# Kernel tuning notes

Measured on AMD Instinct MI355X. Metric: run time of the kernel, lower is better.

Reference implementation:

```python
import jax, jax.numpy as jnp
import numpy as np

C = 10000   # crystals
K = 5       # elements per crystal
N = C * K   # nodes
EMB = 200   # element embedding length
F = 64      # elem_fea_len
L = 3       # n_graph
H = 3       # heads
HID = 256   # gate/msg hidden dim


def setup_inputs() -> dict:
    key = jax.random.key(0)
    ks = jax.random.split(key, 16)
    # structured intra-crystal all-pairs edge lists (grouped by crystal)
    i_loc = np.repeat(np.arange(K), K)
    j_loc = np.tile(np.arange(K), K)
    base = np.arange(C)[:, None] * K
    self_idx = (base + i_loc).ravel().astype(np.int32)   # [M]
    nbr_idx = (base + j_loc).ravel().astype(np.int32)    # [M]
    cry_idx = np.repeat(np.arange(C), K).astype(np.int32)  # [N]
    def nrm(k, shape, s=0.05):
        return jax.random.normal(k, shape, jnp.float32) * s
    return dict(
        elem_weights=jax.random.uniform(ks[0], (N, 1), jnp.float32, 0.05, 1.0),
        elem_fea=jax.random.normal(ks[1], (N, EMB), jnp.float32),
        self_fea_idx=jnp.asarray(self_idx),
        nbr_fea_idx=jnp.asarray(nbr_idx),
        cry_elem_idx=jnp.asarray(cry_idx),
        n_crystals=C,
        emb_W=nrm(ks[2], (EMB, F - 1)), emb_b=jnp.zeros((F - 1,), jnp.float32),
        g_gate_W1=nrm(ks[3], (L, H, 2 * F, HID)), g_gate_b1=jnp.zeros((L, H, HID), jnp.float32),
        g_gate_W2=nrm(ks[4], (L, H, HID, 1)), g_gate_b2=jnp.zeros((L, H, 1), jnp.float32),
        g_msg_W1=nrm(ks[5], (L, H, 2 * F, HID)), g_msg_b1=jnp.zeros((L, H, HID), jnp.float32),
        g_msg_W2=nrm(ks[6], (L, H, HID, F)), g_msg_b2=jnp.zeros((L, H, F), jnp.float32),
        g_pow=jax.random.normal(ks[7], (L, H), jnp.float32),
        c_gate_W1=nrm(ks[8], (H, F, HID)), c_gate_b1=jnp.zeros((H, HID), jnp.float32),
        c_gate_W2=nrm(ks[9], (H, HID, 1)), c_gate_b2=jnp.zeros((H, 1), jnp.float32),
        c_msg_W1=nrm(ks[10], (H, F, HID)), c_msg_b1=jnp.zeros((H, HID), jnp.float32),
        c_msg_W2=nrm(ks[11], (H, HID, F)), c_msg_b2=jnp.zeros((H, F), jnp.float32),
        c_pow=jax.random.normal(ks[12], (H,), jnp.float32),
    )


def _simple(h, W1, b1, W2, b2):
    # SimpleNetwork: Linear -> LeakyReLU -> Linear (one hidden layer, slope 0.01)
    return jax.nn.leaky_relu(h @ W1 + b1, 0.01) @ W2 + b2


def _attn(fea, weights, index, nseg, gW1, gb1, gW2, gb2, mW1, mb1, mW2, mb2, p):
    # WeightedAttention: segment softmax with learned power on weights
    gate = _simple(fea, gW1, gb1, gW2, gb2)                                   # [E,1]
    gate = gate - jax.ops.segment_max(gate, index, num_segments=nseg)[index]
    gate = weights ** p * jnp.exp(gate)
    gate = gate / (jax.ops.segment_sum(gate, index, num_segments=nseg)[index] + 1e-10)
    msg = _simple(fea, mW1, mb1, mW2, mb2)                                    # [E,F]
    return jax.ops.segment_sum(gate * msg, index, num_segments=nseg)          # [nseg,F]


_attn_heads = jax.vmap(_attn, in_axes=(None, None, None, None, 0, 0, 0, 0, 0, 0, 0, 0, 0))


def _forward(elem_weights, elem_fea, self_fea_idx, nbr_fea_idx, cry_elem_idx, n_crystals,
             emb_W, emb_b,
             g_gate_W1, g_gate_b1, g_gate_W2, g_gate_b2,
             g_msg_W1, g_msg_b1, g_msg_W2, g_msg_b2, g_pow,
             c_gate_W1, c_gate_b1, c_gate_W2, c_gate_b2,
             c_msg_W1, c_msg_b1, c_msg_W2, c_msg_b2, c_pow):
    n_nodes = elem_fea.shape[0]
    x = jnp.concatenate([elem_fea @ emb_W + emb_b, elem_weights], axis=1)     # [N,F]
    w_nbr = elem_weights[nbr_fea_idx]                                          # [M,1]
    for l in range(g_pow.shape[0]):  # n_graph message layers
        cat = jnp.concatenate([x[self_fea_idx], x[nbr_fea_idx]], axis=1)      # [M,2F]
        heads = _attn_heads(cat, w_nbr, self_fea_idx, n_nodes,
                            g_gate_W1[l], g_gate_b1[l], g_gate_W2[l], g_gate_b2[l],
                            g_msg_W1[l], g_msg_b1[l], g_msg_W2[l], g_msg_b2[l], g_pow[l])
        x = heads.mean(0) + x
    heads = _attn_heads(x, elem_weights, cry_elem_idx, n_crystals,
                        c_gate_W1, c_gate_b1, c_gate_W2, c_gate_b2,
                        c_msg_W1, c_msg_b1, c_msg_W2, c_msg_b2, c_pow)
    return heads.mean(0)                                                       # [C,F]


def reference(elem_weights, elem_fea, self_fea_idx, nbr_fea_idx, cry_elem_idx, n_crystals,
              emb_W, emb_b,
              g_gate_W1, g_gate_b1, g_gate_W2, g_gate_b2,
              g_msg_W1, g_msg_b1, g_msg_W2, g_msg_b2, g_pow,
              c_gate_W1, c_gate_b1, c_gate_W2, c_gate_b2,
              c_msg_W1, c_msg_b1, c_msg_W2, c_msg_b2, c_pow):
    return _forward(elem_weights, elem_fea, self_fea_idx, nbr_fea_idx, cry_elem_idx, n_crystals,
                    emb_W, emb_b,
                    g_gate_W1, g_gate_b1, g_gate_W2, g_gate_b2,
                    g_msg_W1, g_msg_b1, g_msg_W2, g_msg_b2, g_pow,
                    c_gate_W1, c_gate_b1, c_gate_W2, c_gate_b2,
                    c_msg_W1, c_msg_b1, c_msg_W2, c_msg_b2, c_pow)
```

## Files before the change

kernel.cpp:

```cpp
#include <hip/hip_runtime.h>
#include <hip/hip_bf16.h>

#define K 5
#define F 64
#define EMBD 200
#define HID 256
#define NH 3
#define NL 3

#define CW 3
#define NWN (CW * K)
#define EWE (CW * K * K)
#define ET 5

typedef _Float16 half8 __attribute__((ext_vector_type(8)));
typedef _Float16 h2 __attribute__((ext_vector_type(2)));
typedef _Float16 h4 __attribute__((ext_vector_type(4)));
typedef __fp16 fp16x2 __attribute__((ext_vector_type(2)));
typedef float f32x4 __attribute__((ext_vector_type(4)));

__device__ __forceinline__ float lrelu(float v) { return v >= 0.f ? v : 0.01f * v; }

__device__ __forceinline__ h2 cvt_pk(float a, float b) {
    union { fp16x2 f; h2 h; } u;
    u.f = __builtin_amdgcn_cvt_pkrtz(a, b);
    return u.h;
}

__device__ __forceinline__ half8 lrelu8(half8 t) {
    half8 z = 0;
    half8 p = __builtin_elementwise_max(t, z);
    half8 n = __builtin_elementwise_min(t, z);
    return p + n * (_Float16)0.01f;
}

#define W1SW_ELEMS 589824
#define W2SW_ELEMS 147456
#define CW1_ELEMS   98304
#define CW2_ELEMS   49152
#define WALL_ELEMS (W1SW_ELEMS + W2SW_ELEMS + CW1_ELEMS + CW2_ELEMS)

#define W1L_ELEMS 196608
#define W2L_ELEMS 49152

__global__ __launch_bounds__(256)
void prep_all(const float* __restrict__ gW1, const float* __restrict__ mW1,
              const float* __restrict__ mW2,
              const float* __restrict__ cgW1, const float* __restrict__ cmW1,
              const float* __restrict__ cmW2,
              _Float16* __restrict__ Wall)
{
    int tid = blockIdx.x * 256 + threadIdx.x;
    if (tid >= WALL_ELEMS) return;
    float v;
    if (tid < W1SW_ELEMS) {
        int j = tid & 7, lane = (tid >> 3) & 63;
        int r1 = tid >> 9;
        int ks = r1 & 1, nt = (r1 >> 1) & 3, chunk = (r1 >> 3) & 3;
        int half = (r1 >> 5) & 1, net = (r1 >> 6) & 1, lh = r1 >> 7;
        int q = lane >> 4, n16 = lane & 15;
        const float* src = net ? mW1 : gW1;
        v = src[((size_t)lh * 128 + half * 64 + ks * 32 + q * 8 + j) * 256
                + chunk * 64 + nt * 16 + n16];
    } else if (tid < W1SW_ELEMS + W2SW_ELEMS) {
        int t2 = tid - W1SW_ELEMS;
        int j = t2 & 7, lane = (t2 >> 3) & 63;
        int r1 = t2 >> 9;
        int nt = r1 & 3, ks2 = (r1 >> 2) & 7, lh = r1 >> 5;
        int q = lane >> 4, n16 = lane & 15;
        v = mW2[((size_t)lh * 256 + ks2 * 32 + q * 8 + j) * 64 + nt * 16 + n16];
    } else if (tid < W1SW_ELEMS + W2SW_ELEMS + CW1_ELEMS) {
        int t2 = tid - (W1SW_ELEMS + W2SW_ELEMS);
        int j = t2 & 7, lane = (t2 >> 3) & 63;
        int r1 = t2 >> 9;
        int ks = r1 & 1, nt = (r1 >> 1) & 3, chunk = (r1 >> 3) & 3;
        int net = (r1 >> 5) & 1, h = r1 >> 6;
        int q = lane >> 4, n16 = lane & 15;
        const float* src = net ? cmW1 : cgW1;
        v = src[((size_t)h * 64 + ks * 32 + q * 8 + j) * 256
                + chunk * 64 + nt * 16 + n16];
    } else {
        int t2 = tid - (W1SW_ELEMS + W2SW_ELEMS + CW1_ELEMS);
        int j = t2 & 7, lane = (t2 >> 3) & 63;
        int r1 = t2 >> 9;
        int nt = r1 & 3, ks2 = (r1 >> 2) & 7, h = r1 >> 5;
        int q = lane >> 4, n16 = lane & 15;
        v = cmW2[((size_t)h * 256 + ks2 * 32 + q * 8 + j) * 64 + nt * 16 + n16];
    }
    Wall[tid] = (_Float16)v;
}

__global__ __launch_bounds__(256)
void prep_layer(const float* __restrict__ gW1, const float* __restrict__ mW1,
                const float* __restrict__ mW2,
                _Float16* __restrict__ W1sw, _Float16* __restrict__ W2sw, int l)
{
    int tid = blockIdx.x * 256 + threadIdx.x;
    if (tid < W1L_ELEMS) {
        int j = tid & 7, lane = (tid >> 3) & 63;
        int r1 = tid >> 9;
        int ks = r1 & 1, nt = (r1 >> 1) & 3, chunk = (r1 >> 3) & 3;
        int half = (r1 >> 5) & 1, net = (r1 >> 6) & 1, hh = r1 >> 7;
        int q = lane >> 4, n16 = lane & 15;
        const float* src = net ? mW1 : gW1;
        float v = src[((size_t)(l * NH + hh) * 128 + half * 64 + ks * 32 + q * 8 + j) * 256
                      + chunk * 64 + nt * 16 + n16];
        W1sw[tid] = (_Float16)v;
    } else {
        int t2 = tid - W1L_ELEMS;
        if (t2 < W2L_ELEMS) {
            int j = t2 & 7, lane = (t2 >> 3) & 63;
            int r1 = t2 >> 9;
            int nt = r1 & 3, ks2 = (r1 >> 2) & 7, hh = r1 >> 5;
            int q = lane >> 4, n16 = lane & 15;
            float v = mW2[((size_t)(l * NH + hh) * 256 + ks2 * 32 + q * 8 + j) * 64
                          + nt * 16 + n16];
            W2sw[t2] = (_Float16)v;
        }
    }
}

__global__ __launch_bounds__(64)
void embed_kernel(const float* __restrict__ fea, const float* __restrict__ W,
                  const float* __restrict__ b, const float* __restrict__ wts,
                  float* __restrict__ x)
{
    int n = blockIdx.x;
    int o = threadIdx.x;
    __shared__ float fs[EMBD];
    for (int e = o; e < EMBD; e += 64) fs[e] = fea[n * EMBD + e];
    __syncthreads();
    if (o < F - 1) {
        float acc = b[o];
#pragma unroll 8
        for (int e = 0; e < EMBD; ++e) acc += fs[e] * W[e * (F - 1) + o];
        x[n * F + o] = acc;
    } else {
        x[n * F + F - 1] = wts[n];
    }
}

#define WAVE_LDS 12288

__global__ __launch_bounds__(256, 2)
void net_wave(const float* __restrict__ x,
              const _Float16* __restrict__ W1sw,
              const _Float16* __restrict__ W2sw,
              const float* __restrict__ gb1, const float* __restrict__ gb2v,
              const float* __restrict__ mb1, const float* __restrict__ mb2,
              const float* __restrict__ gW2, const float* __restrict__ gpw,
              const _Float16* __restrict__ cW1sw,
              const _Float16* __restrict__ cW2sw,
              const float* __restrict__ cgb1, const float* __restrict__ cgb2v,
              const float* __restrict__ cmb1, const float* __restrict__ cmb2,
              const float* __restrict__ cgW2, const float* __restrict__ cpw,
              const float* __restrict__ wts, float* __restrict__ out, int Ntot)
{
    __shared__ __align__(16) char smem[4 * WAVE_LDS];

    const int t = threadIdx.x, w = t >> 6, lane = t & 63;
    const int q = lane >> 4, m16 = lane & 15;

    char* wb = smem + w * WAVE_LDS;
    _Float16 (*PQ)[16][72] = (_Float16 (*)[16][72])wb;
    _Float16 (*msgL)[72]   = (_Float16 (*)[72])wb;
    _Float16 (*xS)[72]     = (_Float16 (*)[72])(wb + 9216);
    float* gateS  = (float*)(wb + 11520);
    float* anormS = (float*)(wb + 11840);
    float* wpowS  = (float*)(wb + 12160);

    const int nw0 = (blockIdx.x * 12 + w * CW) * K;
    const int c0  = blockIdx.x * 12 + w * CW;
    const int Ctot = Ntot / K;
    const int vn  = (Ntot - nw0 < NWN) ? (Ntot - nw0) : NWN;
    const int vc  = (Ctot - c0 < CW) ? (Ctot - c0) : CW;
    (void)vn;

    half8 A[2];
    {
        int arow = nw0 + m16;
        if (arow > Ntot - 1) arow = Ntot - 1;
        if (arow < 0) arow = 0;
        const float* xr = x + (size_t)arow * F;
#pragma unroll
        for (int ks = 0; ks < 2; ++ks) {
            float4 f0 = *(const float4*)(xr + ks * 32 + q * 8);
            float4 f1 = *(const float4*)(xr + ks * 32 + q * 8 + 4);
            half8 a;
            a[0] = (_Float16)f0.x; a[1] = (_Float16)f0.y;
            a[2] = (_Float16)f0.z; a[3] = (_Float16)f0.w;
            a[4] = (_Float16)f1.x; a[5] = (_Float16)f1.y;
            a[6] = (_Float16)f1.z; a[7] = (_Float16)f1.w;
            A[ks] = a;
        }
    }

    float xcur[NWN];
#pragma unroll
    for (int n = 0; n < NWN; ++n) {
        int r = nw0 + n;
        if (r > Ntot - 1) r = Ntot - 1;
        if (r < 0) r = 0;
        xcur[n] = x[(size_t)r * F + lane];
    }

    int iR[ET], jR[ET];
#pragma unroll
    for (int et = 0; et < ET; ++et) {
        int e = et * 16 + m16;
        if (e < EWE) {
            int cl = e / 25, rm = e % 25;
            iR[et] = cl * K + rm / K;
            jR[et] = cl * K + rm % K;
        } else { iR[et] = 15; jR[et] = 15; }
    }

#pragma clang loop unroll(disable)
    for (int l = 0; l < NL; ++l) {
        float oacc[NWN];
#pragma unroll
        for (int n = 0; n < NWN; ++n) oacc[n] = 0.f;

        for (int h = 0; h < NH; ++h) {
            const int lh = l * NH + h, lhw = lh;

            if (lane < NWN) {
                int wi = nw0 + lane;
                if (wi > Ntot - 1) wi = Ntot - 1;
                if (wi < 0) wi = 0;
                wpowS[lane] = powf(wts[wi], gpw[lh]);
            }
            if (lane >= NWN && lane < NWN + 5) anormS[EWE + (lane - NWN)] = 0.f;

            f32x4 acc2[ET][4];
#pragma unroll
            for (int et = 0; et < ET; ++et)
#pragma unroll
                for (int nt = 0; nt < 4; ++nt) acc2[et][nt] = (f32x4){0.f, 0.f, 0.f, 0.f};
            float gacc[ET] = {0.f, 0.f, 0.f, 0.f, 0.f};

            for (int c = 0; c < 4; ++c) {
                half8 B2[8];
                {
                    const _Float16* W2b = W2sw + ((size_t)lhw * 8 + c * 2) * 2048;
#pragma unroll
                    for (int f = 0; f < 8; ++f)
                        B2[f] = *(const half8*)(W2b + ((size_t)f * 64 + lane) * 8);
                }

#pragma unroll
                for (int hf = 0; hf < 4; ++hf) {
                    f32x4 accS[4];
#pragma unroll
                    for (int nt = 0; nt < 4; ++nt) accS[nt] = (f32x4){0.f, 0.f, 0.f, 0.f};
                    const _Float16* Wb = W1sw + ((size_t)lhw * 4 + hf) * 16384 + c * 4096;
#pragma unroll
                    for (int nt = 0; nt < 4; ++nt)
#pragma unroll
                        for (int ks = 0; ks < 2; ++ks) {
                            half8 B = *(const half8*)(Wb + ((nt * 2 + ks) * 64 + lane) * 8);
                            accS[nt] = __builtin_amdgcn_mfma_f32_16x16x32_f16(
                                B, A[ks], accS[nt], 0, 0, 0);
                        }
#pragma unroll
                    for (int nt = 0; nt < 4; ++nt) {
                        h2 lo = cvt_pk(accS[nt][0], accS[nt][1]);
                        h2 hi = cvt_pk(accS[nt][2], accS[nt][3]);
                        h4 pk = __builtin_shufflevector(lo, hi, 0, 1, 2, 3);
                        *(h4*)&PQ[hf][m16][nt * 16 + q * 4] = pk;
                    }
                }

                half8 bg8[2], bm8[2];
                h2 wgh2[2][4];
#pragma unroll
                for (int ks = 0; ks < 2; ++ks) {
                    const int ub = c * 64 + ks * 32 + q * 8;
                    float4 g0 = *(const float4*)(gb1 + (size_t)lh * HID + ub);
                    float4 g1 = *(const float4*)(gb1 + (size_t)lh * HID + ub + 4);
                    float4 m0 = *(const float4*)(mb1 + (size_t)lh * HID + ub);
                    float4 m1 = *(const float4*)(mb1 + (size_t)lh * HID + ub + 4);
                    float4 w0 = *(const float4*)(gW2 + (size_t)lh * HID + ub);
                    float4 w1 = *(const float4*)(gW2 + (size_t)lh * HID + ub + 4);
                    half8 bg, bm;
                    bg[0]=(_Float16)g0.x; bg[1]=(_Float16)g0.y; bg[2]=(_Float16)g0.z; bg[3]=(_Float16)g0.w;
                    bg[4]=(_Float16)g1.x; bg[5]=(_Float16)g1.y; bg[6]=(_Float16)g1.z; bg[7]=(_Float16)g1.w;
                    bm[0]=(_Float16)m0.x; bm[1]=(_Float16)m0.y; bm[2]=(_Float16)m0.z; bm[3]=(_Float16)m0.w;
                    bm[4]=(_Float16)m1.x; bm[5]=(_Float16)m1.y; bm[6]=(_Float16)m1.z; bm[7]=(_Float16)m1.w;
                    bg8[ks] = bg; bm8[ks] = bm;
                    wgh2[ks][0] = cvt_pk(w0.x, w0.y);
                    wgh2[ks][1] = cvt_pk(w0.z, w0.w);
                    wgh2[ks][2] = cvt_pk(w1.x, w1.y);
                    wgh2[ks][3] = cvt_pk(w1.z, w1.w);
                }

#pragma unroll
                for (int et = 0; et < ET; ++et) {
                    half8 af[2];
#pragma unroll
                    for (int ks = 0; ks < 2; ++ks) {
                        const int ub = ks * 32 + q * 8;
                        half8 pg = *(const half8*)&PQ[0][iR[et]][ub];
                        half8 qg = *(const half8*)&PQ[1][jR[et]][ub];
                        half8 pm = *(const half8*)&PQ[2][iR[et]][ub];
                        half8 qm = *(const half8*)&PQ[3][jR[et]][ub];
                        half8 tg = lrelu8(pg + qg + bg8[ks]);
                        h2 t01 = __builtin_shufflevector(tg, tg, 0, 1);
                        h2 t23 = __builtin_shufflevector(tg, tg, 2, 3);
                        h2 t45 = __builtin_shufflevector(tg, tg, 4, 5);
                        h2 t67 = __builtin_shufflevector(tg, tg, 6, 7);
                        gacc[et] = __builtin_amdgcn_fdot2(t01, wgh2[ks][0], gacc[et], false);
                        gacc[et] = __builtin_amdgcn_fdot2(t23, wgh2[ks][1], gacc[et], false);
                        gacc[et] = __builtin_amdgcn_fdot2(t45, wgh2[ks][2], gacc[et], false);
                        gacc[et] = __builtin_amdgcn_fdot2(t67, wgh2[ks][3], gacc[et], false);
                        af[ks] = lrelu8(pm + qm + bm8[ks]);
                    }
#pragma unroll
                    for (int nt = 0; nt < 4; ++nt)
#pragma unroll
                        for (int ks = 0; ks < 2; ++ks)
                            acc2[et][nt] = __builtin_amdgcn_mfma_f32_16x16x32_f16(
                                af[ks], B2[ks * 4 + nt], acc2[et][nt], 0, 0, 0);
                }
            }

            const float gb2s = gb2v[lh];
#pragma unroll
            for (int et = 0; et < ET; ++et) {
                float g = gacc[et];
                g += __shfl_xor(g, 16);
                g += __shfl_xor(g, 32);
                if (q == 0) gateS[et * 16 + m16] = g + gb2s;
            }

            if (lane < NWN) {
                const int cl5 = (lane / K) * K;
                float gg[K], mx = -1e30f;
#pragma unroll
                for (int jj = 0; jj < K; ++jj) {
                    gg[jj] = gateS[lane * K + jj];
                    mx = fmaxf(mx, gg[jj]);
                }
                float s = 0.f, wv[K];
#pragma unroll
                for (int jj = 0; jj < K; ++jj) {
                    wv[jj] = wpowS[cl5 + jj] * expf(gg[jj] - mx);
                    s += wv[jj];
                }
                float inv = 1.f / (s + 1e-10f) * (1.f / 3.f);
#pragma unroll
                for (int jj = 0; jj < K; ++jj) anormS[lane * K + jj] = wv[jj] * inv;
            }

            float b2v[4];
#pragma unroll
            for (int nt = 0; nt < 4; ++nt) b2v[nt] = mb2[(size_t)lh * F + nt * 16 + m16];
#pragma unroll
            for (int et = 0; et < ET; ++et) {
                f32x4 an = *(const f32x4*)&anormS[et * 16 + q * 4];
#pragma unroll
                for (int nt = 0; nt < 4; ++nt)
#pragma unroll
                    for (int rg = 0; rg < 4; ++rg) {
                        float v = (acc2[et][nt][rg] + b2v[nt]) * an[rg];
                        msgL[et * 16 + q * 4 + rg][nt * 16 + m16] = (_Float16)v;
                    }
            }

#pragma unroll
            for (int n = 0; n < NWN; ++n) {
                float s = 0.f;
#pragma unroll
                for (int jj = 0; jj < K; ++jj) s += (float)msgL[n * K + jj][lane];
                oacc[n] += s;
            }
        }

#pragma unroll
        for (int n = 0; n < NWN; ++n) {
            float xn = oacc[n] + xcur[n];
            xcur[n] = xn;
            xS[n][lane] = (_Float16)xn;
        }
        xS[15][lane] = (_Float16)0.f;
#pragma unroll
        for (int ks = 0; ks < 2; ++ks)
            A[ks] = *(const half8*)&xS[m16][ks * 32 + q * 8];
    }

    _Float16 (*PQp)[16][72] = (_Float16 (*)[16][72])wb;
    _Float16 (*msgP)[72]    = (_Float16 (*)[72])wb;

    float oaccP[CW] = {0.f, 0.f, 0.f};

    for (int h = 0; h < NH; ++h) {
        if (lane < NWN) {
            int wi = nw0 + lane;
            if (wi > Ntot - 1) wi = Ntot - 1;
            if (wi < 0) wi = 0;
            wpowS[lane] = powf(wts[wi], cpw[h]);
        }
        if (lane == NWN) anormS[15] = 0.f;

        f32x4 acc2[4];
#pragma unroll
        for (int nt = 0; nt < 4; ++nt) acc2[nt] = (f32x4){0.f, 0.f, 0.f, 0.f};
        float gacc = 0.f;

        for (int c = 0; c < 4; ++c) {
            half8 B2[8];
            {
                const _Float16* W2b = cW2sw + (size_t)h * 16384 + c * 4096;
#pragma unroll
                for (int f = 0; f < 8; ++f)
                    B2[f] = *(const half8*)(W2b + ((size_t)f * 64 + lane) * 8);
            }

#pragma unroll
            for (int net = 0; net < 2; ++net) {
                f32x4 accS[4];
#pragma unroll
                for (int nt = 0; nt < 4; ++nt) accS[nt] = (f32x4){0.f, 0.f, 0.f, 0.f};
                const _Float16* Wb = cW1sw + ((size_t)(h * 2 + net) * 4 + c) * 4096;
#pragma unroll
                for (int nt = 0; nt < 4; ++nt)
#pragma unroll
                    for (int ks = 0; ks < 2; ++ks) {
                        half8 B = *(const half8*)(Wb + ((nt * 2 + ks) * 64 + lane) * 8);
                        accS[nt] = __builtin_amdgcn_mfma_f32_16x16x32_f16(
                            B, A[ks], accS[nt], 0, 0, 0);
                    }
#pragma unroll
                for (int nt = 0; nt < 4; ++nt) {
                    h2 lo = cvt_pk(accS[nt][0], accS[nt][1]);
                    h2 hi = cvt_pk(accS[nt][2], accS[nt][3]);
                    h4 pk = __builtin_shufflevector(lo, hi, 0, 1, 2, 3);
                    *(h4*)&PQp[net][m16][nt * 16 + q * 4] = pk;
                }
            }

            half8 bg8[2], bm8[2];
            h2 wgh2[2][4];
#pragma unroll
            for (int ks = 0; ks < 2; ++ks) {
                const int ub = c * 64 + ks * 32 + q * 8;
                float4 g0 = *(const float4*)(cgb1 + (size_t)h * HID + ub);
                float4 g1 = *(const float4*)(cgb1 + (size_t)h * HID + ub + 4);
                float4 m0 = *(const float4*)(cmb1 + (size_t)h * HID + ub);
                float4 m1 = *(const float4*)(cmb1 + (size_t)h * HID + ub + 4);
                float4 w0 = *(const float4*)(cgW2 + (size_t)h * HID + ub);
                float4 w1 = *(const float4*)(cgW2 + (size_t)h * HID + ub + 4);
                half8 bg, bm;
                bg[0]=(_Float16)g0.x; bg[1]=(_Float16)g0.y; bg[2]=(_Float16)g0.z; bg[3]=(_Float16)g0.w;
                bg[4]=(_Float16)g1.x; bg[5]=(_Float16)g1.y; bg[6]=(_Float16)g1.z; bg[7]=(_Float16)g1.w;
                bm[0]=(_Float16)m0.x; bm[1]=(_Float16)m0.y; bm[2]=(_Float16)m0.z; bm[3]=(_Float16)m0.w;
                bm[4]=(_Float16)m1.x; bm[5]=(_Float16)m1.y; bm[6]=(_Float16)m1.z; bm[7]=(_Float16)m1.w;
                bg8[ks] = bg; bm8[ks] = bm;
                wgh2[ks][0] = cvt_pk(w0.x, w0.y);
                wgh2[ks][1] = cvt_pk(w0.z, w0.w);
                wgh2[ks][2] = cvt_pk(w1.x, w1.y);
                wgh2[ks][3] = cvt_pk(w1.z, w1.w);
            }

            {
                half8 af[2];
#pragma unroll
                for (int ks = 0; ks < 2; ++ks) {
                    const int ub = ks * 32 + q * 8;
                    half8 pg = *(const half8*)&PQp[0][m16][ub];
                    half8 pm = *(const half8*)&PQp[1][m16][ub];
                    half8 tg = lrelu8(pg + bg8[ks]);
                    h2 t01 = __builtin_shufflevector(tg, tg, 0, 1);
                    h2 t23 = __builtin_shufflevector(tg, tg, 2, 3);
                    h2 t45 = __builtin_shufflevector(tg, tg, 4, 5);
                    h2 t67 = __builtin_shufflevector(tg, tg, 6, 7);
                    gacc = __builtin_amdgcn_fdot2(t01, wgh2[ks][0], gacc, false);
                    gacc = __builtin_amdgcn_fdot2(t23, wgh2[ks][1], gacc, false);
                    gacc = __builtin_amdgcn_fdot2(t45, wgh2[ks][2], gacc, false);
                    gacc = __builtin_amdgcn_fdot2(t67, wgh2[ks][3], gacc, false);
                    af[ks] = lrelu8(pm + bm8[ks]);
                }
#pragma unroll
                for (int nt = 0; nt < 4; ++nt)
#pragma unroll
                    for (int ks = 0; ks < 2; ++ks)
                        acc2[nt] = __builtin_amdgcn_mfma_f32_16x16x32_f16(
                            af[ks], B2[ks * 4 + nt], acc2[nt], 0, 0, 0);
            }
        }

        const float gb2s = cgb2v[h];
        {
            float g = gacc;
            g += __shfl_xor(g, 16);
            g += __shfl_xor(g, 32);
            if (q == 0) gateS[m16] = g + gb2s;
        }

        if (lane < CW) {
            const int n0 = lane * K;
            float gg[K], mx = -1e30f;
#pragma unroll
            for (int jj = 0; jj < K; ++jj) {
                gg[jj] = gateS[n0 + jj];
                mx = fmaxf(mx, gg[jj]);
            }
            float s = 0.f, wv[K];
#pragma unroll
            for (int jj = 0; jj < K; ++jj) {
                wv[jj] = wpowS[n0 + jj] * expf(gg[jj] - mx);
                s += wv[jj];
            }
            float inv = 1.f / (s + 1e-10f) * (1.f / 3.f);
#pragma unroll
            for (int jj = 0; jj < K; ++jj) anormS[n0 + jj] = wv[jj] * inv;
        }

        float b2v[4];
#pragma unroll
        for (int nt = 0; nt < 4; ++nt) b2v[nt] = cmb2[(size_t)h * F + nt * 16 + m16];
#pragma unroll
        for (int nt = 0; nt < 4; ++nt)
#pragma unroll
            for (int rg = 0; rg < 4; ++rg) {
                int row = q * 4 + rg;
                float v = (acc2[nt][rg] + b2v[nt]) * anormS[row];
                msgP[row][nt * 16 + m16] = (_Float16)v;
            }

#pragma unroll
        for (int cl = 0; cl < CW; ++cl) {
            float s = 0.f;
#pragma unroll
            for (int jj = 0; jj < K; ++jj) s += (float)msgP[cl * K + jj][lane];
            oaccP[cl] += s;
        }
    }

#pragma unroll
    for (int cl = 0; cl < CW; ++cl)
        if (cl < vc)
            out[(size_t)(c0 + cl) * F + lane] = oaccP[cl];
}

__global__ __launch_bounds__(256, 2)
void layer_wave(float* __restrict__ x,
                const _Float16* __restrict__ W1sw,
                const _Float16* __restrict__ W2sw,
                const float* __restrict__ gb1, const float* __restrict__ gb2v,
                const float* __restrict__ mb1, const float* __restrict__ mb2,
                const float* __restrict__ gW2, const float* __restrict__ gpw,
                const float* __restrict__ wts, int l, int lhw0, int Ntot)
{
    __shared__ __align__(16) char smem[4 * WAVE_LDS];

    const int t = threadIdx.x, w = t >> 6, lane = t & 63;
    const int q = lane >> 4, m16 = lane & 15;

    char* wb = smem + w * WAVE_LDS;
    _Float16 (*PQ)[16][72] = (_Float16 (*)[16][72])wb;
    _Float16 (*msgL)[72]   = (_Float16 (*)[72])wb;
    float* gateS  = (float*)(wb + 11520);
    float* anormS = (float*)(wb + 11840);
    float* wpowS  = (float*)(wb + 12160);

    const int nw0 = (blockIdx.x * 12 + w * CW) * K;
    const int vn  = (Ntot - nw0 < NWN) ? (Ntot - nw0) : NWN;

    half8 A[2];
    {
        int arow = nw0 + m16;
        if (arow > Ntot - 1) arow = Ntot - 1;
        if (arow < 0) arow = 0;
        const float* xr = x + (size_t)arow * F;
#pragma unroll
        for (int ks = 0; ks < 2; ++ks) {
            float4 f0 = *(const float4*)(xr + ks * 32 + q * 8);
            float4 f1 = *(const float4*)(xr + ks * 32 + q * 8 + 4);
            half8 a;
            a[0] = (_Float16)f0.x; a[1] = (_Float16)f0.y;
            a[2] = (_Float16)f0.z; a[3] = (_Float16)f0.w;
            a[4] = (_Float16)f1.x; a[5] = (_Float16)f1.y;
            a[6] = (_Float16)f1.z; a[7] = (_Float16)f1.w;
            A[ks] = a;
        }
    }

    int iR[ET], jR[ET];
#pragma unroll
    for (int et = 0; et < ET; ++et) {
        int e = et * 16 + m16;
        if (e < EWE) {
            int cl = e / 25, rm = e % 25;
            iR[et] = cl * K + rm / K;
            jR[et] = cl * K + rm % K;
        } else { iR[et] = 15; jR[et] = 15; }
    }

    float oacc[NWN];
#pragma unroll
    for (int n = 0; n < NWN; ++n) oacc[n] = 0.f;

    for (int h = 0; h < NH; ++h) {
        const int lh = l * NH + h, lhw = lhw0 + h;

        if (lane < NWN) {
            int wi = nw0 + lane;
            if (wi > Ntot - 1) wi = Ntot - 1;
            if (wi < 0) wi = 0;
            wpowS[lane] = powf(wts[wi], gpw[lh]);
        }
        if (lane >= NWN && lane < NWN + 5) anormS[EWE + (lane - NWN)] = 0.f;

        f32x4 acc2[ET][4];
#pragma unroll
        for (int et = 0; et < ET; ++et)
#pragma unroll
            for (int nt = 0; nt < 4; ++nt) acc2[et][nt] = (f32x4){0.f, 0.f, 0.f, 0.f};
        float gacc[ET] = {0.f, 0.f, 0.f, 0.f, 0.f};

        for (int c = 0; c < 4; ++c) {
            half8 B2[8];
            {
                const _Float16* W2b = W2sw + ((size_t)lhw * 8 + c * 2) * 2048;
#pragma unroll
                for (int f = 0; f < 8; ++f)
                    B2[f] = *(const half8*)(W2b + ((size_t)f * 64 + lane) * 8);
            }

#pragma unroll
            for (int hf = 0; hf < 4; ++hf) {
                f32x4 accS[4];
#pragma unroll
                for (int nt = 0; nt < 4; ++nt) accS[nt] = (f32x4){0.f, 0.f, 0.f, 0.f};
                const _Float16* Wb = W1sw + ((size_t)lhw * 4 + hf) * 16384 + c * 4096;
#pragma unroll
                for (int nt = 0; nt < 4; ++nt)
#pragma unroll
                    for (int ks = 0; ks < 2; ++ks) {
                        half8 B = *(const half8*)(Wb + ((nt * 2 + ks) * 64 + lane) * 8);
                        accS[nt] = __builtin_amdgcn_mfma_f32_16x16x32_f16(
                            B, A[ks], accS[nt], 0, 0, 0);
                    }
#pragma unroll
                for (int nt = 0; nt < 4; ++nt) {
                    h2 lo = cvt_pk(accS[nt][0], accS[nt][1]);
                    h2 hi = cvt_pk(accS[nt][2], accS[nt][3]);
                    h4 pk = __builtin_shufflevector(lo, hi, 0, 1, 2, 3);
                    *(h4*)&PQ[hf][m16][nt * 16 + q * 4] = pk;
                }
            }

            half8 bg8[2], bm8[2];
            h2 wgh2[2][4];
#pragma unroll
            for (int ks = 0; ks < 2; ++ks) {
                const int ub = c * 64 + ks * 32 + q * 8;
                float4 g0 = *(const float4*)(gb1 + (size_t)lh * HID + ub);
                float4 g1 = *(const float4*)(gb1 + (size_t)lh * HID + ub + 4);
                float4 m0 = *(const float4*)(mb1 + (size_t)lh * HID + ub);
                float4 m1 = *(const float4*)(mb1 + (size_t)lh * HID + ub + 4);
                float4 w0 = *(const float4*)(gW2 + (size_t)lh * HID + ub);
                float4 w1 = *(const float4*)(gW2 + (size_t)lh * HID + ub + 4);
                half8 bg, bm;
                bg[0]=(_Float16)g0.x; bg[1]=(_Float16)g0.y; bg[2]=(_Float16)g0.z; bg[3]=(_Float16)g0.w;
                bg[4]=(_Float16)g1.x; bg[5]=(_Float16)g1.y; bg[6]=(_Float16)g1.z; bg[7]=(_Float16)g1.w;
                bm[0]=(_Float16)m0.x; bm[1]=(_Float16)m0.y; bm[2]=(_Float16)m0.z; bm[3]=(_Float16)m0.w;
                bm[4]=(_Float16)m1.x; bm[5]=(_Float16)m1.y; bm[6]=(_Float16)m1.z; bm[7]=(_Float16)m1.w;
                bg8[ks] = bg; bm8[ks] = bm;
                wgh2[ks][0] = cvt_pk(w0.x, w0.y);
                wgh2[ks][1] = cvt_pk(w0.z, w0.w);
                wgh2[ks][2] = cvt_pk(w1.x, w1.y);
                wgh2[ks][3] = cvt_pk(w1.z, w1.w);
            }

#pragma unroll
            for (int et = 0; et < ET; ++et) {
                half8 af[2];
#pragma unroll
                for (int ks = 0; ks < 2; ++ks) {
                    const int ub = ks * 32 + q * 8;
                    half8 pg = *(const half8*)&PQ[0][iR[et]][ub];
                    half8 qg = *(const half8*)&PQ[1][jR[et]][ub];
                    half8 pm = *(const half8*)&PQ[2][iR[et]][ub];
                    half8 qm = *(const half8*)&PQ[3][jR[et]][ub];
                    half8 tg = lrelu8(pg + qg + bg8[ks]);
                    h2 t01 = __builtin_shufflevector(tg, tg, 0, 1);
                    h2 t23 = __builtin_shufflevector(tg, tg, 2, 3);
                    h2 t45 = __builtin_shufflevector(tg, tg, 4, 5);
                    h2 t67 = __builtin_shufflevector(tg, tg, 6, 7);
                    gacc[et] = __builtin_amdgcn_fdot2(t01, wgh2[ks][0], gacc[et], false);
                    gacc[et] = __builtin_amdgcn_fdot2(t23, wgh2[ks][1], gacc[et], false);
                    gacc[et] = __builtin_amdgcn_fdot2(t45, wgh2[ks][2], gacc[et], false);
                    gacc[et] = __builtin_amdgcn_fdot2(t67, wgh2[ks][3], gacc[et], false);
                    af[ks] = lrelu8(pm + qm + bm8[ks]);
                }
#pragma unroll
                for (int nt = 0; nt < 4; ++nt)
#pragma unroll
                    for (int ks = 0; ks < 2; ++ks)
                        acc2[et][nt] = __builtin_amdgcn_mfma_f32_16x16x32_f16(
                            af[ks], B2[ks * 4 + nt], acc2[et][nt], 0, 0, 0);
            }
        }

        const float gb2s = gb2v[lh];
#pragma unroll
        for (int et = 0; et < ET; ++et) {
            float g = gacc[et];
            g += __shfl_xor(g, 16);
            g += __shfl_xor(g, 32);
            if (q == 0) gateS[et * 16 + m16] = g + gb2s;
        }

        if (lane < NWN) {
            const int cl5 = (lane / K) * K;
            float gg[K], mx = -1e30f;
#pragma unroll
            for (int jj = 0; jj < K; ++jj) {
                gg[jj] = gateS[lane * K + jj];
                mx = fmaxf(mx, gg[jj]);
            }
            float s = 0.f, wv[K];
#pragma unroll
            for (int jj = 0; jj < K; ++jj) {
                wv[jj] = wpowS[cl5 + jj] * expf(gg[jj] - mx);
                s += wv[jj];
            }
            float inv = 1.f / (s + 1e-10f) * (1.f / 3.f);
#pragma unroll
            for (int jj = 0; jj < K; ++jj) anormS[lane * K + jj] = wv[jj] * inv;
        }

        float b2v[4];
#pragma unroll
        for (int nt = 0; nt < 4; ++nt) b2v[nt] = mb2[(size_t)lh * F + nt * 16 + m16];
#pragma unroll
        for (int et = 0; et < ET; ++et) {
            f32x4 an = *(const f32x4*)&anormS[et * 16 + q * 4];
#pragma unroll
            for (int nt = 0; nt < 4; ++nt)
#pragma unroll
                for (int rg = 0; rg < 4; ++rg) {
                    float v = (acc2[et][nt][rg] + b2v[nt]) * an[rg];
                    msgL[et * 16 + q * 4 + rg][nt * 16 + m16] = (_Float16)v;
                }
        }

#pragma unroll
        for (int n = 0; n < NWN; ++n) {
            float s = 0.f;
#pragma unroll
            for (int jj = 0; jj < K; ++jj) s += (float)msgL[n * K + jj][lane];
            oacc[n] += s;
        }
    }

#pragma unroll
    for (int n = 0; n < NWN; ++n) {
        if (n < vn) {
            size_t idx = (size_t)(nw0 + n) * F + lane;
            x[idx] = oacc[n] + x[idx];
        }
    }
}

__global__ __launch_bounds__(256)
void pool_kernel(const float* __restrict__ x,
                 const float* __restrict__ cgW1, const float* __restrict__ cgb1,
                 const float* __restrict__ cgW2, const float* __restrict__ cgb2,
                 const float* __restrict__ cmW1, const float* __restrict__ cmb1,
                 const float* __restrict__ cmW2, const float* __restrict__ cmb2,
                 const float* __restrict__ cpw, const float* __restrict__ wts,
                 float* __restrict__ out)
{
    __shared__ float xs[K * F];
    __shared__ float hmS[K][HID];
    __shared__ float msgS[K][F];
    __shared__ float outacc[F];
    __shared__ float b1g[HID], b1m[HID], w2g[HID];
    __shared__ float b2mS[F];
    __shared__ float gpart[K][2];
    __shared__ float gate_s[K];
    __shared__ float anorm[K];
    __shared__ float wn[K], wpow[K];

    const int c = blockIdx.x;
    const int t = threadIdx.x;
    const int wave = t >> 6, lane = t & 63;

    for (int d = t; d < K * F; d += 256) xs[d] = x[c * K * F + d];
    if (t < F) outacc[t] = 0.f;
    if (t < K) wn[t] = wts[c * K + t];
    __syncthreads();

    for (int h = 0; h < NH; ++h) {
        if (t < HID) {
            b1g[t] = cgb1[(size_t)h * HID + t];
            b1m[t] = cmb1[(size_t)h * HID + t];
            w2g[t] = cgW2[(size_t)h * HID + t];
        }
        if (t < F) b2mS[t] = cmb2[(size_t)h * F + t];
        if (t < K) wpow[t] = powf(wn[t], cpw[h]);
        __syncthreads();

        {
            const int grp = t >> 7;
            const int up  = t & 127;
            const float* Wb = (grp == 0 ? cgW1 : cmW1) + (size_t)h * F * HID;
            const float2* W2p = (const float2*)Wb;
            float acc[K][2];
#pragma unroll
            for (int i = 0; i < K; ++i) { acc[i][0] = 0.f; acc[i][1] = 0.f; }
            for (int k = 0; k < F; ++k) {
                float2 wv = W2p[k * (HID / 2) + up];
#pragma unroll
                for (int i = 0; i < K; ++i) {
                    float xv = xs[i * F + k];
                    acc[i][0] += xv * wv.x;
                    acc[i][1] += xv * wv.y;
                }
            }
            if (grp == 0) {
#pragma unroll
                for (int i = 0; i < K; ++i) {
                    float h0 = lrelu(acc[i][0] + b1g[2 * up]);
                    float h1 = lrelu(acc[i][1] + b1g[2 * up + 1]);
                    float part = h0 * w2g[2 * up] + h1 * w2g[2 * up + 1];
#pragma unroll
                    for (int s = 32; s; s >>= 1) part += __shfl_xor(part, s);
                    if (lane == 0) gpart[i][wave & 1] = part;
                }
            } else {
#pragma unroll
                for (int i = 0; i < K; ++i) {
                    hmS[i][2 * up]     = lrelu(acc[i][0] + b1m[2 * up]);
                    hmS[i][2 * up + 1] = lrelu(acc[i][1] + b1m[2 * up + 1]);
                }
            }
        }
        __syncthreads();
        if (t < K) gate_s[t] = cgb2[h] + gpart[t][0] + gpart[t][1];

        {
            const float2* W232 = (const float2*)(cmW2 + (size_t)h * HID * F);
            if (t < K * (F / 2)) {
                int i  = t >> 5;
                int op = t & 31;
                float a0 = b2mS[2 * op], a1 = b2mS[2 * op + 1];
#pragma unroll 8
                for (int u = 0; u < HID; ++u) {
                    float2 wv = W232[u * (F / 2) + op];
                    float hv = hmS[i][u];
                    a0 += hv * wv.x;
                    a1 += hv * wv.y;
                }
                msgS[i][2 * op]     = a0;
                msgS[i][2 * op + 1] = a1;
            }
        }
        __syncthreads();

        if (t == 0) {
            float mx = -1e30f;
#pragma unroll
            for (int i = 0; i < K; ++i) mx = fmaxf(mx, gate_s[i]);
            float wv[K], s = 0.f;
#pragma unroll
            for (int i = 0; i < K; ++i) {
                wv[i] = wpow[i] * expf(gate_s[i] - mx);
                s += wv[i];
            }
            float inv = 1.f / (s + 1e-10f);
#pragma unroll
            for (int i = 0; i < K; ++i) anorm[i] = wv[i] * inv;
        }
        __syncthreads();

        if (t < F) {
            float s = 0.f;
#pragma unroll
            for (int i = 0; i < K; ++i) s += anorm[i] * msgS[i][t];
            outacc[t] += s * (1.f / 3.f);
        }
        __syncthreads();
    }

    if (t < F) out[(size_t)c * F + t] = outacc[t];
}

extern "C" void kernel_launch(void* const* d_in, const int* in_sizes, int n_in,
                              void* d_out, int out_size, void* d_ws, size_t ws_size,
                              hipStream_t stream)
{
    const float* wts  = (const float*)d_in[0];
    const float* fea  = (const float*)d_in[1];
    const float* embW = (const float*)d_in[6];
    const float* embB = (const float*)d_in[7];
    const float* gW1  = (const float*)d_in[8];
    const float* gb1  = (const float*)d_in[9];
    const float* gW2  = (const float*)d_in[10];
    const float* gb2  = (const float*)d_in[11];
    const float* mW1  = (const float*)d_in[12];
    const float* mb1  = (const float*)d_in[13];
    const float* mW2  = (const float*)d_in[14];
    const float* mb2  = (const float*)d_in[15];
    const float* gpw  = (const float*)d_in[16];
    const float* cgW1 = (const float*)d_in[17];
    const float* cgb1 = (const float*)d_in[18];
    const float* cgW2 = (const float*)d_in[19];
    const float* cgb2 = (const float*)d_in[20];
    const float* cmW1 = (const float*)d_in[21];
    const float* cmb1 = (const float*)d_in[22];
    const float* cmW2 = (const float*)d_in[23];
    const float* cmb2 = (const float*)d_in[24];
    const float* cpw  = (const float*)d_in[25];

    const int N = in_sizes[0];
    const int C = N / K;
    const int layer_blocks = (C + 11) / 12;

    float* x = (float*)d_ws;
    const size_t xbytes = (size_t)N * F * 4;
    const size_t need = xbytes + (size_t)WALL_ELEMS * 2;

    embed_kernel<<<N, 64, 0, stream>>>(fea, embW, embB, wts, x);

    if (ws_size >= need) {
        _Float16* Wall  = (_Float16*)((char*)d_ws + xbytes);
        _Float16* W1sw  = Wall;
        _Float16* W2sw  = Wall + W1SW_ELEMS;
        _Float16* cW1sw = Wall + W1SW_ELEMS + W2SW_ELEMS;
        _Float16* cW2sw = Wall + W1SW_ELEMS + W2SW_ELEMS + CW1_ELEMS;

        prep_all<<<(WALL_ELEMS + 255) / 256, 256, 0, stream>>>(
            gW1, mW1, mW2, cgW1, cmW1, cmW2, Wall);
        net_wave<<<layer_blocks, 256, 0, stream>>>(
            x, W1sw, W2sw, gb1, gb2, mb1, mb2, gW2, gpw,
            cW1sw, cW2sw, cgb1, cgb2, cmb1, cmb2, cgW2, cpw,
            wts, (float*)d_out, N);
    } else {
        _Float16* W1sw = (_Float16*)d_out;
        _Float16* W2sw = (_Float16*)((char*)d_out + 393216);
        for (int l = 0; l < NL; ++l) {
            prep_layer<<<(W1L_ELEMS + W2L_ELEMS) / 256, 256, 0, stream>>>(
                gW1, mW1, mW2, W1sw, W2sw, l);
            layer_wave<<<layer_blocks, 256, 0, stream>>>(x, W1sw, W2sw,
                                                         gb1, gb2, mb1, mb2, gW2, gpw, wts,
                                                         l, 0, N);
        }
        pool_kernel<<<C, 256, 0, stream>>>(x, cgW1, cgb1, cgW2, cgb2,
                                           cmW1, cmb1, cmW2, cmb2, cpw, wts,
                                           (float*)d_out);
    }
}
```

Measured before the change: 723.1 us.

## Fuse element embedding into net_wave using MFMA with pre-swizzled fp16 weights

Removes the separate embed_kernel launch on the fast path. The embedding matmul (200->63) now runs inside net_wave as fp16 MFMA, with a swizzled embedding weight block produced by prep_all. The result is staged in LDS and read back into the A fragments and xcur. This drops one launch plus the global write and re-read of x, but the embedding inputs now lose precision through fp16 rounding.

```diff
diff --git a/kernel.cpp b/kernel.cpp
--- a/kernel.cpp
+++ b/kernel.cpp
@@ -39,6 +39,8 @@
 #define CW1_ELEMS   98304
 #define CW2_ELEMS   49152
 #define WALL_ELEMS (W1SW_ELEMS + W2SW_ELEMS + CW1_ELEMS + CW2_ELEMS)
+#define EMBSW_ELEMS 14336
+#define WALL2_ELEMS (WALL_ELEMS + EMBSW_ELEMS)
 
 #define W1L_ELEMS 196608
 #define W2L_ELEMS 49152
@@ -47,11 +49,11 @@
 void prep_all(const float* __restrict__ gW1, const float* __restrict__ mW1,
               const float* __restrict__ mW2,
               const float* __restrict__ cgW1, const float* __restrict__ cmW1,
-              const float* __restrict__ cmW2,
+              const float* __restrict__ cmW2, const float* __restrict__ embW,
               _Float16* __restrict__ Wall)
 {
     int tid = blockIdx.x * 256 + threadIdx.x;
-    if (tid >= WALL_ELEMS) return;
+    if (tid >= WALL2_ELEMS) return;
     float v;
     if (tid < W1SW_ELEMS) {
         int j = tid & 7, lane = (tid >> 3) & 63;
@@ -79,13 +81,21 @@
         const float* src = net ? cmW1 : cgW1;
         v = src[((size_t)h * 64 + ks * 32 + q * 8 + j) * 256
                 + chunk * 64 + nt * 16 + n16];
-    } else {
+    } else if (tid < WALL_ELEMS) {
         int t2 = tid - (W1SW_ELEMS + W2SW_ELEMS + CW1_ELEMS);
         int j = t2 & 7, lane = (t2 >> 3) & 63;
         int r1 = t2 >> 9;
         int nt = r1 & 3, ks2 = (r1 >> 2) & 7, h = r1 >> 5;
         int q = lane >> 4, n16 = lane & 15;
         v = cmW2[((size_t)h * 256 + ks2 * 32 + q * 8 + j) * 64 + nt * 16 + n16];
+    } else {
+        int t2 = tid - WALL_ELEMS;
+        int j = t2 & 7, lane = (t2 >> 3) & 63;
+        int r1 = t2 >> 9;
+        int nt = r1 & 3, kk = r1 >> 2;
+        int q = lane >> 4, n16 = lane & 15;
+        int row = kk * 32 + q * 8 + j, col = nt * 16 + n16;
+        v = (row < EMBD && col < F - 1) ? embW[(size_t)row * (F - 1) + col] : 0.f;
     }
     Wall[tid] = (_Float16)v;
 }
@@ -141,9 +151,11 @@
 }
 
 #define WAVE_LDS 12288
+#define XFS 68
 
 __global__ __launch_bounds__(256, 2)
-void net_wave(const float* __restrict__ x,
+void net_wave(const float* __restrict__ fea, const float* __restrict__ embB,
+              const _Float16* __restrict__ embWsw,
               const _Float16* __restrict__ W1sw,
               const _Float16* __restrict__ W2sw,
               const float* __restrict__ gb1, const float* __restrict__ gb2v,
@@ -172,36 +184,60 @@
     const int nw0 = (blockIdx.x * 12 + w * CW) * K;
     const int c0  = blockIdx.x * 12 + w * CW;
     const int Ctot = Ntot / K;
-    const int vn  = (Ntot - nw0 < NWN) ? (Ntot - nw0) : NWN;
     const int vc  = (Ctot - c0 < CW) ? (Ctot - c0) : CW;
-    (void)vn;
-
-    half8 A[2];
+
+    float* xF = (float*)wb;
     {
         int arow = nw0 + m16;
         if (arow > Ntot - 1) arow = Ntot - 1;
         if (arow < 0) arow = 0;
-        const float* xr = x + (size_t)arow * F;
-#pragma unroll
-        for (int ks = 0; ks < 2; ++ks) {
-            float4 f0 = *(const float4*)(xr + ks * 32 + q * 8);
-            float4 f1 = *(const float4*)(xr + ks * 32 + q * 8 + 4);
-            half8 a;
-            a[0] = (_Float16)f0.x; a[1] = (_Float16)f0.y;
-            a[2] = (_Float16)f0.z; a[3] = (_Float16)f0.w;
-            a[4] = (_Float16)f1.x; a[5] = (_Float16)f1.y;
-            a[6] = (_Float16)f1.z; a[7] = (_Float16)f1.w;
-            A[ks] = a;
-        }
+        const float* fr = fea + (size_t)arow * EMBD;
+        f32x4 accE[4];
+#pragma unroll
+        for (int nt = 0; nt < 4; ++nt) accE[nt] = (f32x4){0.f, 0.f, 0.f, 0.f};
+#pragma unroll
+        for (int kk = 0; kk < 7; ++kk) {
+            half8 Bf;
+            if (kk < 6 || q == 0) {
+                float4 f0 = *(const float4*)(fr + kk * 32 + q * 8);
+                float4 f1 = *(const float4*)(fr + kk * 32 + q * 8 + 4);
+                Bf[0]=(_Float16)f0.x; Bf[1]=(_Float16)f0.y;
+                Bf[2]=(_Float16)f0.z; Bf[3]=(_Float16)f0.w;
+                Bf[4]=(_Float16)f1.x; Bf[5]=(_Float16)f1.y;
+                Bf[6]=(_Float16)f1.z; Bf[7]=(_Float16)f1.w;
+            } else Bf = 0;
+#pragma unroll
+            for (int nt = 0; nt < 4; ++nt) {
+                half8 Wf = *(const half8*)(embWsw + ((size_t)(kk * 4 + nt) * 64 + lane) * 8);
+                accE[nt] = __builtin_amdgcn_mfma_f32_16x16x32_f16(Wf, Bf, accE[nt], 0, 0, 0);
+            }
+        }
+        const float wv = wts[arow];
+#pragma unroll
+        for (int nt = 0; nt < 4; ++nt)
+#pragma unroll
+            for (int rg = 0; rg < 4; ++rg) {
+                int o = nt * 16 + q * 4 + rg;
+                float val = accE[nt][rg] + embB[o < F - 1 ? o : F - 2];
+                if (o == F - 1) val = wv;
+                xF[m16 * XFS + o] = val;
+            }
     }
 
     float xcur[NWN];
 #pragma unroll
-    for (int n = 0; n < NWN; ++n) {
-        int r = nw0 + n;
-        if (r > Ntot - 1) r = Ntot - 1;
-        if (r < 0) r = 0;
-        xcur[n] = x[(size_t)r * F + lane];
+    for (int n = 0; n < NWN; ++n) xcur[n] = xF[n * XFS + lane];
+    half8 A[2];
+#pragma unroll
+    for (int ks = 0; ks < 2; ++ks) {
+        float4 f0 = *(const float4*)&xF[m16 * XFS + ks * 32 + q * 8];
+        float4 f1 = *(const float4*)&xF[m16 * XFS + ks * 32 + q * 8 + 4];
+        half8 a;
+        a[0] = (_Float16)f0.x; a[1] = (_Float16)f0.y;
+        a[2] = (_Float16)f0.z; a[3] = (_Float16)f0.w;
+        a[4] = (_Float16)f1.x; a[5] = (_Float16)f1.y;
+        a[6] = (_Float16)f1.z; a[7] = (_Float16)f1.w;
+        A[ks] = a;
     }
 
     int iR[ET], jR[ET];
@@ -922,9 +958,7 @@
 
     float* x = (float*)d_ws;
     const size_t xbytes = (size_t)N * F * 4;
-    const size_t need = xbytes + (size_t)WALL_ELEMS * 2;
-
-    embed_kernel<<<N, 64, 0, stream>>>(fea, embW, embB, wts, x);
+    const size_t need = xbytes + (size_t)WALL2_ELEMS * 2;
 
     if (ws_size >= need) {
         _Float16* Wall  = (_Float16*)((char*)d_ws + xbytes);
@@ -932,14 +966,16 @@
         _Float16* W2sw  = Wall + W1SW_ELEMS;
         _Float16* cW1sw = Wall + W1SW_ELEMS + W2SW_ELEMS;
         _Float16* cW2sw = Wall + W1SW_ELEMS + W2SW_ELEMS + CW1_ELEMS;
-
-        prep_all<<<(WALL_ELEMS + 255) / 256, 256, 0, stream>>>(
-            gW1, mW1, mW2, cgW1, cmW1, cmW2, Wall);
+        _Float16* eWsw  = Wall + WALL_ELEMS;
+
+        prep_all<<<(WALL2_ELEMS + 255) / 256, 256, 0, stream>>>(
+            gW1, mW1, mW2, cgW1, cmW1, cmW2, embW, Wall);
         net_wave<<<layer_blocks, 256, 0, stream>>>(
-            x, W1sw, W2sw, gb1, gb2, mb1, mb2, gW2, gpw,
+            fea, embB, eWsw, W1sw, W2sw, gb1, gb2, mb1, mb2, gW2, gpw,
             cW1sw, cW2sw, cgb1, cgb2, cmb1, cmb2, cgW2, cpw,
             wts, (float*)d_out, N);
     } else {
+        embed_kernel<<<N, 64, 0, stream>>>(fea, embW, embB, wts, x);
         _Float16* W1sw = (_Float16*)d_out;
         _Float16* W2sw = (_Float16*)((char*)d_out + 393216);
         for (int l = 0; l < NL; ++l) {
```

Result: faster. 675.6 us (-6.6%).
